# Kernel optimization log

Hardware: AMD Instinct MI355X
Metric: run time of the kernel (lower is better)

## Reference

```python
import jax, jax.numpy as jnp
import numpy as np

N_NODES = 100000
N_EDGES = 1600000
IN_CH = 128
HID = 128
N_GRAPHS = 512


def setup_inputs() -> dict:
    key = jax.random.key(0)
    ks = jax.random.split(key, 16)
    x = jax.random.normal(ks[0], (N_NODES, IN_CH), dtype=jnp.float32)
    edge_index = jax.random.randint(ks[1], (2, N_EDGES), 0, N_NODES, dtype=jnp.int64)
    batch = jnp.sort(jax.random.randint(ks[2], (N_NODES,), 0, N_GRAPHS, dtype=jnp.int64))
    s = 1.0 / np.sqrt(HID)
    params = {
        'W1': jax.random.normal(ks[3], (IN_CH, HID), jnp.float32) / np.sqrt(IN_CH),
        'b1': jnp.zeros((HID,), jnp.float32),
        'W2': jax.random.normal(ks[4], (HID, HID), jnp.float32) * s,
        'b2': jnp.zeros((HID,), jnp.float32),
        'W3': jax.random.normal(ks[5], (HID, HID), jnp.float32) * s,
        'b3': jnp.zeros((HID,), jnp.float32),
        'Wf1': jax.random.normal(ks[6], (2 * HID, HID), jnp.float32) / np.sqrt(2 * HID),
        'bf1': jnp.zeros((HID,), jnp.float32),
        'Wf2': jax.random.normal(ks[7], (HID, HID // 2), jnp.float32) * s,
        'bf2': jnp.zeros((HID // 2,), jnp.float32),
        'Wf3': jax.random.normal(ks[8], (HID // 2, 1), jnp.float32) / np.sqrt(HID // 2),
        'bf3': jnp.zeros((1,), jnp.float32),
    }
    return {'x': x, 'edge_index': edge_index, 'batch': batch, 'n_graphs': N_GRAPHS, **params}


def _gcn_norm(edge_index, n_nodes):
    # add self-loops, then symmetric normalization D^{-1/2} (A+I) D^{-1/2}
    loops = jnp.arange(n_nodes, dtype=edge_index.dtype)
    src = jnp.concatenate([edge_index[0], loops])
    dst = jnp.concatenate([edge_index[1], loops])
    deg = jax.ops.segment_sum(jnp.ones_like(dst, dtype=jnp.float32), dst, num_segments=n_nodes)
    dinv = jnp.where(deg > 0, jax.lax.rsqrt(deg), 0.0)
    norm = dinv[src] * dinv[dst]  # [E + N]
    return src, dst, norm


def _gcn_conv(h, W, b, src, dst, norm, n_nodes):
    h = h @ W                                   # [N, H]
    msg = h[src] * norm[:, None]                # gather + edge scale
    agg = jax.ops.segment_sum(msg, dst, num_segments=n_nodes)  # scatter-add
    return agg + b


def reference(x, edge_index, batch, n_graphs, W1, b1, W2, b2, W3, b3, Wf1, bf1, Wf2, bf2, Wf3, bf3):
    n_nodes = x.shape[0]
    src, dst, norm = _gcn_norm(edge_index, n_nodes)

    h = jax.nn.relu(_gcn_conv(x, W1, b1, src, dst, norm, n_nodes))
    h_res = h
    h = jax.nn.relu(_gcn_conv(h, W2, b2, src, dst, norm, n_nodes)) + h_res
    h_res = h
    h = jax.nn.relu(_gcn_conv(h, W3, b3, src, dst, norm, n_nodes)) + h_res

    ones = jnp.ones((n_nodes, 1), jnp.float32)
    counts = jax.ops.segment_sum(ones, batch, num_segments=n_graphs)  # [G,1]
    g_mean = jax.ops.segment_sum(h, batch, num_segments=n_graphs) / jnp.maximum(counts, 1.0)
    g_max = jax.ops.segment_max(h, batch, num_segments=n_graphs)
    g = jnp.concatenate([g_mean, g_max], axis=1)  # [G, 2H]

    # MLP head (dropout is identity at inference)
    g = jax.nn.relu(g @ Wf1 + bf1)
    g = jax.nn.relu(g @ Wf2 + bf2)
    return g @ Wf3 + bf3  # [G, 1]
```

## Files before the change

### kernel.cpp

```cpp
#include <hip/hip_runtime.h>
#include <hip/hip_bf16.h>

#define NBMAX 128

typedef __attribute__((ext_vector_type(8))) short short8;
typedef __attribute__((ext_vector_type(4))) float f32x4;

__device__ inline unsigned short bf16_rne(float x) {
    unsigned u = __float_as_uint(x);
    u = (u + 0x7FFFu + ((u >> 16) & 1u)) >> 16;
    return (unsigned short)u;
}
__device__ inline float bf16_to_f(unsigned short h) {
    return __uint_as_float(((unsigned)h) << 16);
}
__device__ inline void split2(float v, short& h, short& lo) {
    unsigned short hb = bf16_rne(v);
    h = (short)hb;
    lo = (short)bf16_rne(v - bf16_to_f(hb));
}
__device__ inline float4 unpack_bf16_quad(uint2 q) {
    float4 r;
    r.x = __uint_as_float(q.x << 16);
    r.y = __uint_as_float(q.x & 0xFFFF0000u);
    r.z = __uint_as_float(q.y << 16);
    r.w = __uint_as_float(q.y & 0xFFFF0000u);
    return r;
}


__global__ __launch_bounds__(256) void k_bcnt(const int* __restrict__ dst, int E, int NB,
                                              int* __restrict__ bucket_cnt) {
    __shared__ int lcnt[NBMAX];
    int t = threadIdx.x;
    int base = blockIdx.x * 4096;
    for (int i = t; i < NB; i += 256) lcnt[i] = 0;
    __syncthreads();
#pragma unroll
    for (int i = 0; i < 16; i++) {
        int e = base + i * 256 + t;
        if (e < E) atomicAdd(&lcnt[dst[e] >> 10], 1);
    }
    __syncthreads();
    for (int i = t; i < NB; i += 256) {
        int c = lcnt[i];
        if (c) atomicAdd(&bucket_cnt[i], c);
    }
}

__global__ __launch_bounds__(128) void k_bscan(const int* __restrict__ bucket_cnt,
                                               int NB, int E, int N,
                                               int* __restrict__ bucket_off,
                                               int* __restrict__ bcur,
                                               int* __restrict__ rowstart) {
    __shared__ int sh[128];
    int t = threadIdx.x;
    int v = (t < NB) ? bucket_cnt[t] : 0;
    sh[t] = v;
    __syncthreads();
    for (int off = 1; off < 128; off <<= 1) {
        int x = (t >= off) ? sh[t - off] : 0;
        __syncthreads();
        sh[t] += x;
        __syncthreads();
    }
    if (t < NB) {
        int excl = sh[t] - v;
        bucket_off[t] = excl;
        bcur[t] = excl;
    }
    if (t == 0) {
        bucket_off[NB] = E;
        rowstart[N] = E;
    }
}

__global__ __launch_bounds__(256) void k_bucket(const int* __restrict__ src,
                                                const int* __restrict__ dst, int E, int NB,
                                                int* __restrict__ bcur,
                                                uint2* __restrict__ pairs) {
    __shared__ int lcnt[NBMAX];
    __shared__ int gbase[NBMAX];
    int t = threadIdx.x;
    int base = blockIdx.x * 4096;
    for (int i = t; i < NB; i += 256) lcnt[i] = 0;
    __syncthreads();
    int rank[16];
#pragma unroll
    for (int i = 0; i < 16; i++) {
        int e = base + i * 256 + t;
        rank[i] = (e < E) ? atomicAdd(&lcnt[dst[e] >> 10], 1) : -1;
    }
    __syncthreads();
    for (int i = t; i < NB; i += 256) {
        int c = lcnt[i];
        gbase[i] = c ? atomicAdd(&bcur[i], c) : 0;
    }
    __syncthreads();
#pragma unroll
    for (int i = 0; i < 16; i++) {
        int e = base + i * 256 + t;
        if (e < E) {
            int d = dst[e];
            pairs[gbase[d >> 10] + rank[i]] = make_uint2((unsigned)src[e], (unsigned)d);
        }
    }
}

__global__ __launch_bounds__(1024) void k_node(const uint2* __restrict__ pairs,
                                               const int* __restrict__ bucket_off, int N,
                                               int* __restrict__ rowstart,
                                               float* __restrict__ dinv,
                                               int* __restrict__ csr_src) {
    __shared__ int cnt_l[1024];
    __shared__ int cur_l[1024];
    int t = threadIdx.x;
    int b = blockIdx.x;
    int n0 = b << 10;
    int nn = min(1024, N - n0);
    cnt_l[t] = 0;
    __syncthreads();
    int e0 = bucket_off[b], e1 = bucket_off[b + 1];
    for (int e = e0 + t; e < e1; e += 1024) {
        atomicAdd(&cnt_l[(int)pairs[e].y - n0], 1);
    }
    __syncthreads();
    int c = cnt_l[t];
    for (int off = 1; off < 1024; off <<= 1) {
        int x = (t >= off) ? cnt_l[t - off] : 0;
        __syncthreads();
        cnt_l[t] += x;
        __syncthreads();
    }
    int start = e0 + cnt_l[t] - c;
    cur_l[t] = start;
    if (t < nn) {
        rowstart[n0 + t] = start;
        dinv[n0 + t] = rsqrtf((float)c + 1.0f);
    }
    __syncthreads();
    for (int e = e0 + t; e < e1; e += 1024) {
        uint2 p = pairs[e];
        int r = atomicAdd(&cur_l[(int)p.y - n0], 1);
        csr_src[r] = (int)p.x;
    }
}

__global__ __launch_bounds__(256) void k_wprep(const float* __restrict__ W,
                                               unsigned short* __restrict__ WH,
                                               unsigned short* __restrict__ WL) {
    int idx = blockIdx.x * 256 + threadIdx.x;
    int j = idx & 7;
    int lane = (idx >> 3) & 63;
    int ct = (idx >> 9) & 7;
    int kc = idx >> 12;
    int k = kc * 32 + (lane >> 4) * 8 + j;
    int col = ct * 16 + (lane & 15);
    float v = W[k * 128 + col];
    unsigned short hb = bf16_rne(v);
    WH[idx] = hb;
    WL[idx] = bf16_rne(v - bf16_to_f(hb));
}


__global__ __launch_bounds__(256) void k_gemm3(const float* __restrict__ A,
                                               const unsigned short* __restrict__ WH,
                                               const unsigned short* __restrict__ WL,
                                               const float* __restrict__ dinv,
                                               unsigned short* __restrict__ U, int N) {
    int wv = threadIdx.x >> 6;
    int l = threadIdx.x & 63;
    int quad = l >> 4;
    int lm = l & 15;
    int rowBase = blockIdx.x * 128 + wv * 32;

    f32x4 acc[2][8] = {};

    int r0 = rowBase + lm;
    int r1 = rowBase + 16 + lm;

    for (int kc = 0; kc < 4; kc++) {
        int k0 = kc * 32 + quad * 8;
        float av0[8] = {}, av1[8] = {};
        if (r0 < N) {
            float4 a = *(const float4*)&A[(size_t)r0 * 128 + k0];
            float4 b = *(const float4*)&A[(size_t)r0 * 128 + k0 + 4];
            av0[0] = a.x; av0[1] = a.y; av0[2] = a.z; av0[3] = a.w;
            av0[4] = b.x; av0[5] = b.y; av0[6] = b.z; av0[7] = b.w;
        }
        if (r1 < N) {
            float4 a = *(const float4*)&A[(size_t)r1 * 128 + k0];
            float4 b = *(const float4*)&A[(size_t)r1 * 128 + k0 + 4];
            av1[0] = a.x; av1[1] = a.y; av1[2] = a.z; av1[3] = a.w;
            av1[4] = b.x; av1[5] = b.y; av1[6] = b.z; av1[7] = b.w;
        }
        short8 ah0, al0, ah1, al1;
#pragma unroll
        for (int j = 0; j < 8; j++) {
            short h, lo;
            split2(av0[j], h, lo); ah0[j] = h; al0[j] = lo;
            split2(av1[j], h, lo); ah1[j] = h; al1[j] = lo;
        }
#pragma unroll
        for (int ct = 0; ct < 8; ct++) {
            size_t fo = ((size_t)(kc * 8 + ct) * 64 + l) * 8;
            short8 wh = *(const short8*)&WH[fo];
            short8 wl = *(const short8*)&WL[fo];
            acc[0][ct] = __builtin_amdgcn_mfma_f32_16x16x32_bf16(ah0, wh, acc[0][ct], 0, 0, 0);
            acc[0][ct] = __builtin_amdgcn_mfma_f32_16x16x32_bf16(ah0, wl, acc[0][ct], 0, 0, 0);
            acc[0][ct] = __builtin_amdgcn_mfma_f32_16x16x32_bf16(al0, wh, acc[0][ct], 0, 0, 0);
            acc[1][ct] = __builtin_amdgcn_mfma_f32_16x16x32_bf16(ah1, wh, acc[1][ct], 0, 0, 0);
            acc[1][ct] = __builtin_amdgcn_mfma_f32_16x16x32_bf16(ah1, wl, acc[1][ct], 0, 0, 0);
            acc[1][ct] = __builtin_amdgcn_mfma_f32_16x16x32_bf16(al1, wh, acc[1][ct], 0, 0, 0);
        }
    }

#pragma unroll
    for (int rt = 0; rt < 2; rt++) {
#pragma unroll
        for (int reg = 0; reg < 4; reg++) {
            int row = rowBase + rt * 16 + quad * 4 + reg;
            if (row < N) {
                float dv = dinv[row];
#pragma unroll
                for (int ct = 0; ct < 8; ct++) {
                    U[(size_t)row * 128 + ct * 16 + lm] = bf16_rne(dv * acc[rt][ct][reg]);
                }
            }
        }
    }
}


template <int RES>
__global__ __launch_bounds__(256) void k_agg(const unsigned short* __restrict__ U,
                                             const int* __restrict__ rowstart,
                                             const int* __restrict__ csr_src,
                                             const float* __restrict__ dinv,
                                             const float* __restrict__ bias,
                                             float* __restrict__ H, int N) {
    int wave = threadIdx.x >> 6;
    int lane = threadIdx.x & 63;
    int n = blockIdx.x * 4 + wave;
    if (n >= N) return;
    int g = lane >> 5;
    int l = lane & 31;
    int e0 = rowstart[n], e1 = rowstart[n + 1];
    int half = (e1 - e0) >> 1;
    int a0 = g ? (e0 + half) : e0;
    int a1 = g ? e1 : (e0 + half);

    float4 A0 = {0.f, 0.f, 0.f, 0.f};
    float4 A1 = {0.f, 0.f, 0.f, 0.f};
    float4 A2 = {0.f, 0.f, 0.f, 0.f};
    float4 A3 = {0.f, 0.f, 0.f, 0.f};

    int e = a0;
    for (; e + 4 <= a1; e += 4) {
        int s0 = csr_src[e], s1 = csr_src[e + 1];
        int s2 = csr_src[e + 2], s3 = csr_src[e + 3];
        uint2 q0 = *(const uint2*)&U[(size_t)s0 * 128 + l * 4];
        uint2 q1 = *(const uint2*)&U[(size_t)s1 * 128 + l * 4];
        uint2 q2 = *(const uint2*)&U[(size_t)s2 * 128 + l * 4];
        uint2 q3 = *(const uint2*)&U[(size_t)s3 * 128 + l * 4];
        float4 r0 = unpack_bf16_quad(q0);
        float4 r1 = unpack_bf16_quad(q1);
        float4 r2 = unpack_bf16_quad(q2);
        float4 r3 = unpack_bf16_quad(q3);
        A0.x += r0.x; A0.y += r0.y; A0.z += r0.z; A0.w += r0.w;
        A1.x += r1.x; A1.y += r1.y; A1.z += r1.z; A1.w += r1.w;
        A2.x += r2.x; A2.y += r2.y; A2.z += r2.z; A2.w += r2.w;
        A3.x += r3.x; A3.y += r3.y; A3.z += r3.z; A3.w += r3.w;
    }
    for (; e < a1; e++) {
        int s = csr_src[e];
        uint2 q = *(const uint2*)&U[(size_t)s * 128 + l * 4];
        float4 r = unpack_bf16_quad(q);
        A0.x += r.x; A0.y += r.y; A0.z += r.z; A0.w += r.w;
    }

    float ax = (A0.x + A1.x) + (A2.x + A3.x);
    float ay = (A0.y + A1.y) + (A2.y + A3.y);
    float az = (A0.z + A1.z) + (A2.z + A3.z);
    float aw = (A0.w + A1.w) + (A2.w + A3.w);

    ax += __shfl_xor(ax, 32);
    ay += __shfl_xor(ay, 32);
    az += __shfl_xor(az, 32);
    aw += __shfl_xor(aw, 32);

    if (g == 0) {
        uint2 qs = *(const uint2*)&U[(size_t)n * 128 + l * 4];
        float4 self = unpack_bf16_quad(qs);
        float4 bi = *(const float4*)&bias[l * 4];
        float dn = dinv[n];
        float4 out;
        out.x = fmaxf(dn * (ax + self.x) + bi.x, 0.f);
        out.y = fmaxf(dn * (ay + self.y) + bi.y, 0.f);
        out.z = fmaxf(dn * (az + self.z) + bi.z, 0.f);
        out.w = fmaxf(dn * (aw + self.w) + bi.w, 0.f);
        if (RES) {
            float4 h = *(const float4*)&H[(size_t)n * 128 + l * 4];
            out.x += h.x; out.y += h.y; out.z += h.z; out.w += h.w;
        }
        *(float4*)&H[(size_t)n * 128 + l * 4] = out;
    }
}


__global__ __launch_bounds__(256) void k_gstart(const int* __restrict__ batch, int N, int G,
                                                int* __restrict__ gstart) {
    int g = blockIdx.x * 256 + threadIdx.x;
    if (g > G) return;
    if (g == G) { gstart[g] = N; return; }
    int lo = 0, hi = N;
    while (lo < hi) {
        int mid = (lo + hi) >> 1;
        if (batch[mid] < g) lo = mid + 1; else hi = mid;
    }
    gstart[g] = lo;
}

__global__ __launch_bounds__(256) void k_pool(const float* __restrict__ H,
                                              const int* __restrict__ gstart,
                                              float* __restrict__ gfeat) {
    __shared__ float ssum[256];
    __shared__ float smax[256];
    int g = blockIdx.x;
    int c = threadIdx.x & 127;
    int half = threadIdx.x >> 7;
    int i0 = gstart[g], i1 = gstart[g + 1];
    int cn = i1 - i0;
    int mid = i0 + (cn >> 1);
    int a0 = half ? mid : i0;
    int a1 = half ? i1 : mid;
    float s = 0.f, m = -3.4e38f;
    for (int i = a0; i < a1; i++) {
        float v = H[(size_t)i * 128 + c];
        s += v;
        m = fmaxf(m, v);
    }
    ssum[threadIdx.x] = s;
    smax[threadIdx.x] = m;
    __syncthreads();
    if (half == 0) {
        float st = ssum[c] + ssum[c + 128];
        float mt = fmaxf(smax[c], smax[c + 128]);
        float mean = (cn > 0) ? st / (float)cn : 0.f;
        if (cn == 0) mt = 0.f;
        gfeat[g * 256 + c] = mean;
        gfeat[g * 256 + 128 + c] = mt;
    }
}


__global__ __launch_bounds__(128) void k_mlp(const float* __restrict__ gfeat,
                                             const float* __restrict__ Wf1,
                                             const float* __restrict__ bf1,
                                             const float* __restrict__ Wf2,
                                             const float* __restrict__ bf2,
                                             const float* __restrict__ Wf3,
                                             const float* __restrict__ bf3,
                                             float* __restrict__ out) {
    __shared__ float grow[256];
    __shared__ float o1[128];
    __shared__ float o2[64];
    int g = blockIdx.x;
    int t = threadIdx.x;
    grow[t] = gfeat[g * 256 + t];
    grow[t + 128] = gfeat[g * 256 + 128 + t];
    __syncthreads();
    float acc = bf1[t];
#pragma unroll 8
    for (int k = 0; k < 256; k++) acc = fmaf(grow[k], Wf1[k * 128 + t], acc);
    o1[t] = fmaxf(acc, 0.f);
    __syncthreads();
    if (t < 64) {
        float a2 = bf2[t];
#pragma unroll 8
        for (int k = 0; k < 128; k++) a2 = fmaf(o1[k], Wf2[k * 64 + t], a2);
        o2[t] = fmaxf(a2, 0.f);
    }
    __syncthreads();
    if (t < 64) {
        float p = o2[t] * Wf3[t];
        for (int off = 32; off > 0; off >>= 1) p += __shfl_down(p, off);
        if (t == 0) out[g] = p + bf3[0];
    }
}


extern "C" void kernel_launch(void* const* d_in, const int* in_sizes, int n_in,
                              void* d_out, int out_size, void* d_ws, size_t ws_size,
                              hipStream_t stream) {
    const float* x = (const float*)d_in[0];
    const int* ei = (const int*)d_in[1];
    const int* batch = (const int*)d_in[2];
    const float* W1 = (const float*)d_in[4];
    const float* b1 = (const float*)d_in[5];
    const float* W2 = (const float*)d_in[6];
    const float* b2 = (const float*)d_in[7];
    const float* W3 = (const float*)d_in[8];
    const float* b3 = (const float*)d_in[9];
    const float* Wf1 = (const float*)d_in[10];
    const float* bf1 = (const float*)d_in[11];
    const float* Wf2 = (const float*)d_in[12];
    const float* bf2 = (const float*)d_in[13];
    const float* Wf3 = (const float*)d_in[14];
    const float* bf3 = (const float*)d_in[15];

    const int N = in_sizes[0] / 128;
    const int E = in_sizes[1] / 2;
    const int G = out_size;

    const int* src = ei;
    const int* dst = ei + E;

    char* w = (char*)d_ws;
    size_t off = 0;
    auto alloc = [&](size_t bytes) -> void* {
        void* p = w + off;
        off += (bytes + 255) / 256 * 256;
        return p;
    };
    unsigned short* U = (unsigned short*)alloc((size_t)N * 128 * 2);
    float* H = (float*)alloc((size_t)N * 128 * 4);
    uint2* pairs = (uint2*)alloc((size_t)E * 8);
    int* csr_src = (int*)alloc((size_t)E * 4);
    int* rowstart = (int*)alloc((size_t)(N + 1) * 4);
    float* dinv = (float*)alloc((size_t)N * 4);
    int* bucket_cnt = (int*)alloc(NBMAX * 4);
    int* bucket_off = (int*)alloc((NBMAX + 1) * 4);
    int* bcur = (int*)alloc(NBMAX * 4);
    int* gstart = (int*)alloc((size_t)(G + 1) * 4);
    float* gfeat = (float*)alloc((size_t)G * 256 * 4);
    unsigned short* WHb[3], *WLb[3];
    for (int i = 0; i < 3; i++) {
        WHb[i] = (unsigned short*)alloc(16384 * 2);
        WLb[i] = (unsigned short*)alloc(16384 * 2);
    }
    float* out = (float*)d_out;

    const int NB = (N + 1023) >> 10;
    const int ebk = (E + 4095) / 4096;

    hipMemsetAsync(bucket_cnt, 0, NBMAX * 4, stream);

    k_wprep<<<dim3(64), dim3(256), 0, stream>>>(W1, WHb[0], WLb[0]);
    k_wprep<<<dim3(64), dim3(256), 0, stream>>>(W2, WHb[1], WLb[1]);
    k_wprep<<<dim3(64), dim3(256), 0, stream>>>(W3, WHb[2], WLb[2]);

    k_bcnt<<<dim3(ebk), dim3(256), 0, stream>>>(dst, E, NB, bucket_cnt);
    k_bscan<<<dim3(1), dim3(128), 0, stream>>>(bucket_cnt, NB, E, N, bucket_off, bcur, rowstart);
    k_bucket<<<dim3(ebk), dim3(256), 0, stream>>>(src, dst, E, NB, bcur, pairs);
    k_node<<<dim3(NB), dim3(1024), 0, stream>>>(pairs, bucket_off, N, rowstart, dinv, csr_src);

    const int gemmGrid = (N + 127) / 128;
    const int aggGrid = (N + 3) / 4;

    k_gemm3<<<dim3(gemmGrid), dim3(256), 0, stream>>>(x, WHb[0], WLb[0], dinv, U, N);
    k_agg<0><<<dim3(aggGrid), dim3(256), 0, stream>>>(U, rowstart, csr_src, dinv, b1, H, N);
    k_gemm3<<<dim3(gemmGrid), dim3(256), 0, stream>>>(H, WHb[1], WLb[1], dinv, U, N);
    k_agg<1><<<dim3(aggGrid), dim3(256), 0, stream>>>(U, rowstart, csr_src, dinv, b2, H, N);
    k_gemm3<<<dim3(gemmGrid), dim3(256), 0, stream>>>(H, WHb[2], WLb[2], dinv, U, N);
    k_agg<1><<<dim3(aggGrid), dim3(256), 0, stream>>>(U, rowstart, csr_src, dinv, b3, H, N);

    k_gstart<<<dim3((G + 256) / 256), dim3(256), 0, stream>>>(batch, N, G, gstart);
    k_pool<<<dim3(G), dim3(256), 0, stream>>>(H, gstart, gfeat);
    k_mlp<<<dim3(G), dim3(128), 0, stream>>>(gfeat, Wf1, bf1, Wf2, bf2, Wf3, bf3, out);
}
```

Measured before the change: 535.3 us.

## Split aggregation into channel halves, fuse head kernels, merge prep launches, warp-scan CSR

Each aggregation pass becomes two launches, each covering 64 channels with 4-byte gathers and 8-way unrolled edge loads. The aim is a smaller gathered working set per pass (12.8MB of bf16 rows) that fits better in cache, at the cost of reading the CSR index arrays twice. The three weight-prep kernels and the memset are merged into one launch. The pooling, graph-start search and MLP kernels are fused into one head kernel. The block scan in k_node now uses wave shuffles instead of a barrier-heavy shared-memory loop.

New measurement: 687.8 us. 1.29x slower.

```diff
diff --git a/kernel.cpp b/kernel.cpp
--- a/kernel.cpp
+++ b/kernel.cpp
@@ -18,14 +18,6 @@
     unsigned short hb = bf16_rne(v);
     h = (short)hb;
     lo = (short)bf16_rne(v - bf16_to_f(hb));
-}
-__device__ inline float4 unpack_bf16_quad(uint2 q) {
-    float4 r;
-    r.x = __uint_as_float(q.x << 16);
-    r.y = __uint_as_float(q.x & 0xFFFF0000u);
-    r.z = __uint_as_float(q.y << 16);
-    r.w = __uint_as_float(q.y & 0xFFFF0000u);
-    return r;
 }
 
 
@@ -114,7 +106,9 @@
                                                int* __restrict__ csr_src) {
     __shared__ int cnt_l[1024];
     __shared__ int cur_l[1024];
+    __shared__ int wsum[16];
     int t = threadIdx.x;
+    int lane = t & 63, wv = t >> 6;
     int b = blockIdx.x;
     int n0 = b << 10;
     int nn = min(1024, N - n0);
@@ -126,13 +120,26 @@
     }
     __syncthreads();
     int c = cnt_l[t];
-    for (int off = 1; off < 1024; off <<= 1) {
-        int x = (t >= off) ? cnt_l[t - off] : 0;
-        __syncthreads();
-        cnt_l[t] += x;
-        __syncthreads();
-    }
-    int start = e0 + cnt_l[t] - c;
+    int v = c;
+#pragma unroll
+    for (int off = 1; off < 64; off <<= 1) {
+        int x = __shfl_up(v, off);
+        if (lane >= off) v += x;
+    }
+    if (lane == 63) wsum[wv] = v;
+    __syncthreads();
+    if (wv == 0 && lane < 16) {
+        int wval = wsum[lane];
+#pragma unroll
+        for (int off = 1; off < 16; off <<= 1) {
+            int x = __shfl_up(wval, off);
+            if (lane >= off) wval += x;
+        }
+        wsum[lane] = wval;
+    }
+    __syncthreads();
+    int prefix = (wv > 0) ? wsum[wv - 1] : 0;
+    int start = e0 + prefix + v - c;
     cur_l[t] = start;
     if (t < nn) {
         rowstart[n0 + t] = start;
@@ -146,10 +153,16 @@
     }
 }
 
-__global__ __launch_bounds__(256) void k_wprep(const float* __restrict__ W,
-                                               unsigned short* __restrict__ WH,
-                                               unsigned short* __restrict__ WL) {
-    int idx = blockIdx.x * 256 + threadIdx.x;
+__global__ __launch_bounds__(256) void k_wprep3(const float* __restrict__ W1,
+                                                const float* __restrict__ W2,
+                                                const float* __restrict__ W3,
+                                                unsigned short* __restrict__ WH,
+                                                unsigned short* __restrict__ WL,
+                                                int* __restrict__ bucket_cnt) {
+    if (blockIdx.x == 0 && threadIdx.x < NBMAX) bucket_cnt[threadIdx.x] = 0;
+    int wi = blockIdx.x >> 6;
+    int idx = (blockIdx.x & 63) * 256 + threadIdx.x;
+    const float* W = (wi == 0) ? W1 : (wi == 1) ? W2 : W3;
     int j = idx & 7;
     int lane = (idx >> 3) & 63;
     int ct = (idx >> 9) & 7;
@@ -158,8 +171,8 @@
     int col = ct * 16 + (lane & 15);
     float v = W[k * 128 + col];
     unsigned short hb = bf16_rne(v);
-    WH[idx] = hb;
-    WL[idx] = bf16_rne(v - bf16_to_f(hb));
+    WH[wi * 16384 + idx] = hb;
+    WL[wi * 16384 + idx] = bf16_rne(v - bf16_to_f(hb));
 }
 
 
@@ -233,103 +246,101 @@
 
 
 template <int RES>
-__global__ __launch_bounds__(256) void k_agg(const unsigned short* __restrict__ U,
-                                             const int* __restrict__ rowstart,
-                                             const int* __restrict__ csr_src,
-                                             const float* __restrict__ dinv,
-                                             const float* __restrict__ bias,
-                                             float* __restrict__ H, int N) {
+__global__ __launch_bounds__(256) void k_aggh(const unsigned short* __restrict__ U,
+                                              const int* __restrict__ rowstart,
+                                              const int* __restrict__ csr_src,
+                                              const float* __restrict__ dinv,
+                                              const float* __restrict__ bias,
+                                              float* __restrict__ H, int N, int chOff) {
     int wave = threadIdx.x >> 6;
     int lane = threadIdx.x & 63;
     int n = blockIdx.x * 4 + wave;
     if (n >= N) return;
     int g = lane >> 5;
     int l = lane & 31;
+    const unsigned short* Ub = U + chOff;
     int e0 = rowstart[n], e1 = rowstart[n + 1];
     int half = (e1 - e0) >> 1;
     int a0 = g ? (e0 + half) : e0;
     int a1 = g ? e1 : (e0 + half);
 
-    float4 A0 = {0.f, 0.f, 0.f, 0.f};
-    float4 A1 = {0.f, 0.f, 0.f, 0.f};
-    float4 A2 = {0.f, 0.f, 0.f, 0.f};
-    float4 A3 = {0.f, 0.f, 0.f, 0.f};
+    float2 acc[8];
+#pragma unroll
+    for (int j = 0; j < 8; j++) acc[j] = make_float2(0.f, 0.f);
 
     int e = a0;
-    for (; e + 4 <= a1; e += 4) {
-        int s0 = csr_src[e], s1 = csr_src[e + 1];
-        int s2 = csr_src[e + 2], s3 = csr_src[e + 3];
-        uint2 q0 = *(const uint2*)&U[(size_t)s0 * 128 + l * 4];
-        uint2 q1 = *(const uint2*)&U[(size_t)s1 * 128 + l * 4];
-        uint2 q2 = *(const uint2*)&U[(size_t)s2 * 128 + l * 4];
-        uint2 q3 = *(const uint2*)&U[(size_t)s3 * 128 + l * 4];
-        float4 r0 = unpack_bf16_quad(q0);
-        float4 r1 = unpack_bf16_quad(q1);
-        float4 r2 = unpack_bf16_quad(q2);
-        float4 r3 = unpack_bf16_quad(q3);
-        A0.x += r0.x; A0.y += r0.y; A0.z += r0.z; A0.w += r0.w;
-        A1.x += r1.x; A1.y += r1.y; A1.z += r1.z; A1.w += r1.w;
-        A2.x += r2.x; A2.y += r2.y; A2.z += r2.z; A2.w += r2.w;
-        A3.x += r3.x; A3.y += r3.y; A3.z += r3.z; A3.w += r3.w;
+    for (; e + 8 <= a1; e += 8) {
+        int s[8];
+#pragma unroll
+        for (int j = 0; j < 8; j++) s[j] = csr_src[e + j];
+        unsigned q[8];
+#pragma unroll
+        for (int j = 0; j < 8; j++) q[j] = *(const unsigned*)&Ub[(size_t)s[j] * 128 + l * 2];
+#pragma unroll
+        for (int j = 0; j < 8; j++) {
+            acc[j].x += __uint_as_float(q[j] << 16);
+            acc[j].y += __uint_as_float(q[j] & 0xFFFF0000u);
+        }
     }
     for (; e < a1; e++) {
         int s = csr_src[e];
-        uint2 q = *(const uint2*)&U[(size_t)s * 128 + l * 4];
-        float4 r = unpack_bf16_quad(q);
-        A0.x += r.x; A0.y += r.y; A0.z += r.z; A0.w += r.w;
-    }
-
-    float ax = (A0.x + A1.x) + (A2.x + A3.x);
-    float ay = (A0.y + A1.y) + (A2.y + A3.y);
-    float az = (A0.z + A1.z) + (A2.z + A3.z);
-    float aw = (A0.w + A1.w) + (A2.w + A3.w);
-
-    ax += __shfl_xor(ax, 32);
-    ay += __shfl_xor(ay, 32);
-    az += __shfl_xor(az, 32);
-    aw += __shfl_xor(aw, 32);
+        unsigned q = *(const unsigned*)&Ub[(size_t)s * 128 + l * 2];
+        acc[0].x += __uint_as_float(q << 16);
+        acc[0].y += __uint_as_float(q & 0xFFFF0000u);
+    }
+
+    float sx = ((acc[0].x + acc[1].x) + (acc[2].x + acc[3].x)) +
+               ((acc[4].x + acc[5].x) + (acc[6].x + acc[7].x));
+    float sy = ((acc[0].y + acc[1].y) + (acc[2].y + acc[3].y)) +
+               ((acc[4].y + acc[5].y) + (acc[6].y + acc[7].y));
+
+    sx += __shfl_xor(sx, 32);
+    sy += __shfl_xor(sy, 32);
 
     if (g == 0) {
-        uint2 qs = *(const uint2*)&U[(size_t)n * 128 + l * 4];
-        float4 self = unpack_bf16_quad(qs);
-        float4 bi = *(const float4*)&bias[l * 4];
+        unsigned qs = *(const unsigned*)&Ub[(size_t)n * 128 + l * 2];
+        float2 bi = *(const float2*)&bias[chOff + l * 2];
         float dn = dinv[n];
-        float4 out;
-        out.x = fmaxf(dn * (ax + self.x) + bi.x, 0.f);
-        out.y = fmaxf(dn * (ay + self.y) + bi.y, 0.f);
-        out.z = fmaxf(dn * (az + self.z) + bi.z, 0.f);
-        out.w = fmaxf(dn * (aw + self.w) + bi.w, 0.f);
+        float2 o;
+        o.x = fmaxf(dn * (sx + __uint_as_float(qs << 16)) + bi.x, 0.f);
+        o.y = fmaxf(dn * (sy + __uint_as_float(qs & 0xFFFF0000u)) + bi.y, 0.f);
+        size_t hi = (size_t)n * 128 + chOff + l * 2;
         if (RES) {
-            float4 h = *(const float4*)&H[(size_t)n * 128 + l * 4];
-            out.x += h.x; out.y += h.y; out.z += h.z; out.w += h.w;
-        }
-        *(float4*)&H[(size_t)n * 128 + l * 4] = out;
-    }
-}
-
-
-__global__ __launch_bounds__(256) void k_gstart(const int* __restrict__ batch, int N, int G,
-                                                int* __restrict__ gstart) {
-    int g = blockIdx.x * 256 + threadIdx.x;
-    if (g > G) return;
-    if (g == G) { gstart[g] = N; return; }
-    int lo = 0, hi = N;
-    while (lo < hi) {
-        int mid = (lo + hi) >> 1;
-        if (batch[mid] < g) lo = mid + 1; else hi = mid;
-    }
-    gstart[g] = lo;
-}
-
-__global__ __launch_bounds__(256) void k_pool(const float* __restrict__ H,
-                                              const int* __restrict__ gstart,
-                                              float* __restrict__ gfeat) {
+            float2 h = *(const float2*)&H[hi];
+            o.x += h.x; o.y += h.y;
+        }
+        *(float2*)&H[hi] = o;
+    }
+}
+
+
+__global__ __launch_bounds__(256) void k_head(const float* __restrict__ H,
+                                              const int* __restrict__ batch, int N, int G,
+                                              const float* __restrict__ Wf1,
+                                              const float* __restrict__ bf1,
+                                              const float* __restrict__ Wf2,
+                                              const float* __restrict__ bf2,
+                                              const float* __restrict__ Wf3,
+                                              const float* __restrict__ bf3,
+                                              float* __restrict__ out) {
     __shared__ float ssum[256];
     __shared__ float smax[256];
+    __shared__ float grow[256];
+    __shared__ float o1[128];
+    __shared__ float o2[64];
     int g = blockIdx.x;
-    int c = threadIdx.x & 127;
-    int half = threadIdx.x >> 7;
-    int i0 = gstart[g], i1 = gstart[g + 1];
+    int t = threadIdx.x;
+    int i0, i1;
+    {
+        int lo = 0, hi = N;
+        while (lo < hi) { int m = (lo + hi) >> 1; if (batch[m] < g) lo = m + 1; else hi = m; }
+        i0 = lo;
+        lo = i0; hi = N;
+        while (lo < hi) { int m = (lo + hi) >> 1; if (batch[m] < g + 1) lo = m + 1; else hi = m; }
+        i1 = lo;
+    }
+    int c = t & 127;
+    int half = t >> 7;
     int cn = i1 - i0;
     int mid = i0 + (cn >> 1);
     int a0 = half ? mid : i0;
@@ -340,40 +351,22 @@
         s += v;
         m = fmaxf(m, v);
     }
-    ssum[threadIdx.x] = s;
-    smax[threadIdx.x] = m;
+    ssum[t] = s;
+    smax[t] = m;
     __syncthreads();
     if (half == 0) {
         float st = ssum[c] + ssum[c + 128];
         float mt = fmaxf(smax[c], smax[c + 128]);
-        float mean = (cn > 0) ? st / (float)cn : 0.f;
-        if (cn == 0) mt = 0.f;
-        gfeat[g * 256 + c] = mean;
-        gfeat[g * 256 + 128 + c] = mt;
-    }
-}
-
-
-__global__ __launch_bounds__(128) void k_mlp(const float* __restrict__ gfeat,
-                                             const float* __restrict__ Wf1,
-                                             const float* __restrict__ bf1,
-                                             const float* __restrict__ Wf2,
-                                             const float* __restrict__ bf2,
-                                             const float* __restrict__ Wf3,
-                                             const float* __restrict__ bf3,
-                                             float* __restrict__ out) {
-    __shared__ float grow[256];
-    __shared__ float o1[128];
-    __shared__ float o2[64];
-    int g = blockIdx.x;
-    int t = threadIdx.x;
-    grow[t] = gfeat[g * 256 + t];
-    grow[t + 128] = gfeat[g * 256 + 128 + t];
-    __syncthreads();
-    float acc = bf1[t];
+        grow[c] = (cn > 0) ? st / (float)cn : 0.f;
+        grow[128 + c] = (cn > 0) ? mt : 0.f;
+    }
+    __syncthreads();
+    if (t < 128) {
+        float acc = bf1[t];
 #pragma unroll 8
-    for (int k = 0; k < 256; k++) acc = fmaf(grow[k], Wf1[k * 128 + t], acc);
-    o1[t] = fmaxf(acc, 0.f);
+        for (int k = 0; k < 256; k++) acc = fmaf(grow[k], Wf1[k * 128 + t], acc);
+        o1[t] = fmaxf(acc, 0.f);
+    }
     __syncthreads();
     if (t < 64) {
         float a2 = bf2[t];
@@ -432,23 +425,14 @@
     int* bucket_cnt = (int*)alloc(NBMAX * 4);
     int* bucket_off = (int*)alloc((NBMAX + 1) * 4);
     int* bcur = (int*)alloc(NBMAX * 4);
-    int* gstart = (int*)alloc((size_t)(G + 1) * 4);
-    float* gfeat = (float*)alloc((size_t)G * 256 * 4);
-    unsigned short* WHb[3], *WLb[3];
-    for (int i = 0; i < 3; i++) {
-        WHb[i] = (unsigned short*)alloc(16384 * 2);
-        WLb[i] = (unsigned short*)alloc(16384 * 2);
-    }
+    unsigned short* WH = (unsigned short*)alloc(3 * 16384 * 2);
+    unsigned short* WL = (unsigned short*)alloc(3 * 16384 * 2);
     float* out = (float*)d_out;
 
     const int NB = (N + 1023) >> 10;
     const int ebk = (E + 4095) / 4096;
 
-    hipMemsetAsync(bucket_cnt, 0, NBMAX * 4, stream);
-
-    k_wprep<<<dim3(64), dim3(256), 0, stream>>>(W1, WHb[0], WLb[0]);
-    k_wprep<<<dim3(64), dim3(256), 0, stream>>>(W2, WHb[1], WLb[1]);
-    k_wprep<<<dim3(64), dim3(256), 0, stream>>>(W3, WHb[2], WLb[2]);
+    k_wprep3<<<dim3(192), dim3(256), 0, stream>>>(W1, W2, W3, WH, WL, bucket_cnt);
 
     k_bcnt<<<dim3(ebk), dim3(256), 0, stream>>>(dst, E, NB, bucket_cnt);
     k_bscan<<<dim3(1), dim3(128), 0, stream>>>(bucket_cnt, NB, E, N, bucket_off, bcur, rowstart);
@@ -458,14 +442,15 @@
     const int gemmGrid = (N + 127) / 128;
     const int aggGrid = (N + 3) / 4;
 
-    k_gemm3<<<dim3(gemmGrid), dim3(256), 0, stream>>>(x, WHb[0], WLb[0], dinv, U, N);
-    k_agg<0><<<dim3(aggGrid), dim3(256), 0, stream>>>(U, rowstart, csr_src, dinv, b1, H, N);
-    k_gemm3<<<dim3(gemmGrid), dim3(256), 0, stream>>>(H, WHb[1], WLb[1], dinv, U, N);
-    k_agg<1><<<dim3(aggGrid), dim3(256), 0, stream>>>(U, rowstart, csr_src, dinv, b2, H, N);
-    k_gemm3<<<dim3(gemmGrid), dim3(256), 0, stream>>>(H, WHb[2], WLb[2], dinv, U, N);
-    k_agg<1><<<dim3(aggGrid), dim3(256), 0, stream>>>(U, rowstart, csr_src, dinv, b3, H, N);
-
-    k_gstart<<<dim3((G + 256) / 256), dim3(256), 0, stream>>>(batch, N, G, gstart);
-    k_pool<<<dim3(G), dim3(256), 0, stream>>>(H, gstart, gfeat);
-    k_mlp<<<dim3(G), dim3(128), 0, stream>>>(gfeat, Wf1, bf1, Wf2, bf2, Wf3, bf3, out);
-}
+    k_gemm3<<<dim3(gemmGrid), dim3(256), 0, stream>>>(x, WH, WL, dinv, U, N);
+    k_aggh<0><<<dim3(aggGrid), dim3(256), 0, stream>>>(U, rowstart, csr_src, dinv, b1, H, N, 0);
+    k_aggh<0><<<dim3(aggGrid), dim3(256), 0, stream>>>(U, rowstart, csr_src, dinv, b1, H, N, 64);
+    k_gemm3<<<dim3(gemmGrid), dim3(256), 0, stream>>>(H, WH + 16384, WL + 16384, dinv, U, N);
+    k_aggh<1><<<dim3(aggGrid), dim3(256), 0, stream>>>(U, rowstart, csr_src, dinv, b2, H, N, 0);
+    k_aggh<1><<<dim3(aggGrid), dim3(256), 0, stream>>>(U, rowstart, csr_src, dinv, b2, H, N, 64);
+    k_gemm3<<<dim3(gemmGrid), dim3(256), 0, stream>>>(H, WH + 32768, WL + 32768, dinv, U, N);
+    k_aggh<1><<<dim3(aggGrid), dim3(256), 0, stream>>>(U, rowstart, csr_src, dinv, b3, H, N, 0);
+    k_aggh<1><<<dim3(aggGrid), dim3(256), 0, stream>>>(U, rowstart, csr_src, dinv, b3, H, N, 64);
+
+    k_head<<<dim3(G), dim3(256), 0, stream>>>(H, batch, N, G, Wf1, bf1, Wf2, bf2, Wf3, bf3, out);
+}
```
